# Optimization experiments

Hardware: AMD Instinct MI355X
Metric: run time of the kernel (lower is better)

Reference implementation:

```python
import jax, jax.numpy as jnp
import numpy as np

# YOLOv4 stride-8 head config (yolov4.cfg)
ALL_ANCHORS = [[12,16],[19,36],[40,28],[36,75],[76,55],[72,146],[142,110],[192,243],[459,401]]
ANCHOR_MASK = [0, 1, 2]
N_CLASSES = 80
SCALE_XY = 1.2  # scale_x_y for this head
N_BBOX_ATTRS = 5  # tx, ty, tw, th, obj


def setup_inputs() -> dict:
    key = jax.random.key(0)
    attrs = N_CLASSES + N_BBOX_ATTRS  # 85
    n_anchors = len(ANCHOR_MASK)      # 3
    # raw conv output: [batch, n_anchors*attrs, grid, grid]
    x = jax.random.normal(key, (16, n_anchors * attrs, 76, 76), dtype=jnp.float32)
    return {"x": x, "input_dim": 608}


def reference(x, input_dim):
    B = x.shape[0]
    G = x.shape[2]                      # grid_dim (INPUT_H_DIM)
    stride = input_dim // G             # grid_stride
    A = len(ANCHOR_MASK)
    attrs = N_CLASSES + N_BBOX_ATTRS

    # anchors scaled to grid units: [A, 2]
    anc = jnp.asarray([ALL_ANCHORS[i] for i in ANCHOR_MASK], dtype=jnp.float32) / stride

    # [B, A, attrs, H, W] -> [B, H, W, A, attrs]
    x = x.reshape(B, A, attrs, G, G).transpose(0, 3, 4, 1, 2)

    # yolo_transform: sigmoid+scale tx/ty, exp*anchor tw/th, sigmoid obj+cls
    txy = jax.nn.sigmoid(x[..., 0:2]) * SCALE_XY - (SCALE_XY - 1.0) / 2.0
    twh = jnp.exp(x[..., 2:4]) * anc            # broadcast over [B,H,W,A,2]
    objcls = jax.nn.sigmoid(x[..., 4:])

    # add_grid_offsets: torch.meshgrid(grid, grid) is 'ij' -> y_offset[i,j]=i, x_offset[i,j]=j
    gy, gx = jnp.meshgrid(jnp.arange(G), jnp.arange(G), indexing="ij")
    off = jnp.stack([gx, gy], axis=-1).astype(jnp.float32)[:, :, None, :]  # [H,W,1,2]
    txy = txy + off

    # scale bbox attrs (tx..th) to input-image pixels
    boxes = jnp.concatenate([txy, twh], axis=-1) * jnp.float32(stride)

    out = jnp.concatenate([boxes, objcls], axis=-1)  # [B,H,W,A,attrs]
    return out.reshape(B, G * G * A, attrs)
```

## Files before the change

### kernel.cpp

```cpp
#include <hip/hip_runtime.h>

#define GRIDD  76
#define NROWS  255
#define GG     (GRIDD * GRIDD)
#define QROWS  64
#define QQ     (QROWS * 19)
#define QDW    (QROWS * GRIDD)

typedef __attribute__((address_space(3))) unsigned lds_u32;
typedef __attribute__((address_space(1))) unsigned glb_u32;

__device__ __forceinline__ void gll16(const float* g, float* l) {
    __builtin_amdgcn_global_load_lds((const glb_u32*)g, (lds_u32*)l, 16, 0, 0);
}

__global__ __launch_bounds__(256, 8) void yolo_head_kernel(
    const float* __restrict__ x, const int* __restrict__ dimp,
    float* __restrict__ out)
{
    __shared__ float buf[QDW];
    const unsigned lb    = (blockIdx.x & 7u) * 608u + (blockIdx.x >> 3);
    const unsigned b     = lb / 304u;
    const unsigned hq    = lb - b * 304u;
    const unsigned h     = hq >> 2;
    const unsigned q     = hq & 3u;
    const unsigned rbase = (q == 3u) ? 191u : (q << 6);
    const unsigned t     = threadIdx.x;
    const unsigned wid   = t >> 6;
    const unsigned lane  = t & 63u;
    const float stride   = (float)(*dimp / GRIDD);
    const float fh       = (float)h;

    const float* __restrict__ src = x + (size_t)(b * NROWS + rbase) * GG + h * GRIDD;
    #pragma unroll
    for (unsigned k = 0; k < 5u; ++k) {
        unsigned i = k * 256u + (wid << 6) + lane;
        if (i < QQ) {
            unsigned row = i / 19u;
            unsigned qc  = i - row * 19u;
            gll16(src + (size_t)row * GG + (qc << 2),
                  buf + (size_t)(k * 256u + (wid << 6)) * 4u);
        }
    }
    __syncthreads();

    const unsigned rem  = rbase + lane;
    const unsigned a    = (rem >= 170u) ? 2u : ((rem >= 85u) ? 1u : 0u);
    const unsigned attr = rem - a * 85u;
    const bool  wh  = (attr == 2u) | (attr == 3u);
    const bool  isx = (attr == 0u);
    float anc = 0.f;
    if (attr == 2u) anc = (a == 0u) ? 12.f : ((a == 1u) ? 19.f : 40.f);
    if (attr == 3u) anc = (a == 0u) ? 16.f : ((a == 1u) ? 36.f : 28.f);
    const float mB    = -0.1f * stride;
    const float slog  = wh ? 1.44269504f : -1.44269504f;
    const float A2    = wh ? anc : ((attr < 2u) ? 1.2f * stride : 1.f);
    const float wsel  = isx ? stride : 0.f;
    const float basef = (attr == 1u) ? fmaf(fh, stride, mB) : (isx ? mB : 0.f);
    float* __restrict__ dst = out + (size_t)(b * GRIDD + h) * (GRIDD * NROWS) + rem;

    #pragma unroll
    for (unsigned j = 0; j < 5u; ++j) {
        const unsigned tt = wid + (j << 2);
        if (tt < 19u) {
            const float4 vv = *reinterpret_cast<const float4*>(
                buf + (size_t)lane * GRIDD + (tt << 2));
            #pragma unroll
            for (unsigned i = 0; i < 4u; ++i) {
                const float v  = (i == 0) ? vv.x : (i == 1) ? vv.y : (i == 2) ? vv.z : vv.w;
                const float uf = (float)((tt << 2) + i);
                const float e2 = exp2f(v * slog);
                const float sg = __builtin_amdgcn_rcpf(1.0f + e2);
                const float qv = wh ? e2 : sg;
                const float o  = fmaf(qv, A2, fmaf(uf, wsel, basef));
                dst[(size_t)((tt << 2) + i) * NROWS] = o;
            }
        }
    }
}

extern "C" void kernel_launch(void* const* d_in, const int* in_sizes, int n_in,
                              void* d_out, int out_size, void* d_ws, size_t ws_size,
                              hipStream_t stream) {
    const float* x  = (const float*)d_in[0];
    const int* dimp = (const int*)d_in[1];
    float* out      = (float*)d_out;
    const int B = in_sizes[0] / (NROWS * GG);
    yolo_head_kernel<<<B * GRIDD * 4, 256, 0, stream>>>(x, dimp, out);
}
```

Baseline: 32.96 us.

## Make blocks persistent with double-buffered async LDS staging across rows

Replaces one-block-per-(batch,row,quarter) with 1024 persistent blocks of 512 threads. Each block walks a contiguous range of batch-rows and double-buffers the global-to-LDS loads, so the next row's load overlaps the current row's compute and stores. Synchronization uses raw s_waitcnt/s_barrier asm. This removes per-block launch and load-latency stalls, but relies on exact vmcnt accounting, and the number of rows per block is uneven.

```diff
diff --git a/kernel.cpp b/kernel.cpp
--- a/kernel.cpp
+++ b/kernel.cpp
@@ -4,8 +4,8 @@
 #define NROWS  255
 #define GG     (GRIDD * GRIDD)
 #define QROWS  64
-#define QQ     (QROWS * 19)
 #define QDW    (QROWS * GRIDD)
+#define NGRP   256
 
 typedef __attribute__((address_space(3))) unsigned lds_u32;
 typedef __attribute__((address_space(1))) unsigned glb_u32;
@@ -14,41 +14,50 @@
     __builtin_amdgcn_global_load_lds((const glb_u32*)g, (lds_u32*)l, 16, 0, 0);
 }
 
-__global__ __launch_bounds__(256, 8) void yolo_head_kernel(
+__device__ __forceinline__ void stage_q(const float* __restrict__ src,
+                                        float* buf, unsigned wid, unsigned lane)
+{
+    #pragma unroll
+    for (unsigned k = 0; k < 2u; ++k) {
+        unsigned i   = k * 512u + (wid << 6) + lane;
+        unsigned row = i / 19u;
+        unsigned qc  = i - row * 19u;
+        gll16(src + (size_t)row * GG + (qc << 2),
+              buf + (size_t)(k * 512u + (wid << 6)) * 4u);
+    }
+    {
+        unsigned i = 1024u + wid * 24u + lane;
+        if (lane < 24u) {
+            unsigned row = i / 19u;
+            unsigned qc  = i - row * 19u;
+            gll16(src + (size_t)row * GG + (qc << 2),
+                  buf + (size_t)(1024u + wid * 24u) * 4u);
+        }
+    }
+}
+
+__global__ __launch_bounds__(512, 8) void yolo_head_kernel(
     const float* __restrict__ x, const int* __restrict__ dimp,
-    float* __restrict__ out)
+    float* __restrict__ out, int nbh)
 {
-    __shared__ float buf[QDW];
-    const unsigned lb    = (blockIdx.x & 7u) * 608u + (blockIdx.x >> 3);
-    const unsigned b     = lb / 304u;
-    const unsigned hq    = lb - b * 304u;
-    const unsigned h     = hq >> 2;
-    const unsigned q     = hq & 3u;
+    __shared__ float buf[2][QDW];
+    const unsigned g     = blockIdx.x & 255u;
+    const unsigned q     = blockIdx.x >> 8;
     const unsigned rbase = (q == 3u) ? 191u : (q << 6);
     const unsigned t     = threadIdx.x;
     const unsigned wid   = t >> 6;
     const unsigned lane  = t & 63u;
     const float stride   = (float)(*dimp / GRIDD);
-    const float fh       = (float)h;
-
-    const float* __restrict__ src = x + (size_t)(b * NROWS + rbase) * GG + h * GRIDD;
-    #pragma unroll
-    for (unsigned k = 0; k < 5u; ++k) {
-        unsigned i = k * 256u + (wid << 6) + lane;
-        if (i < QQ) {
-            unsigned row = i / 19u;
-            unsigned qc  = i - row * 19u;
-            gll16(src + (size_t)row * GG + (qc << 2),
-                  buf + (size_t)(k * 256u + (wid << 6)) * 4u);
-        }
-    }
-    __syncthreads();
+    const unsigned bh0 = (g * (unsigned)nbh) >> 8;
+    const unsigned bh1 = ((g + 1u) * (unsigned)nbh) >> 8;
+    const unsigned n   = bh1 - bh0;
 
     const unsigned rem  = rbase + lane;
     const unsigned a    = (rem >= 170u) ? 2u : ((rem >= 85u) ? 1u : 0u);
     const unsigned attr = rem - a * 85u;
-    const bool  wh  = (attr == 2u) | (attr == 3u);
-    const bool  isx = (attr == 0u);
+    const bool  wh   = (attr == 2u) | (attr == 3u);
+    const bool  isx  = (attr == 0u);
+    const bool  isy  = (attr == 1u);
     float anc = 0.f;
     if (attr == 2u) anc = (a == 0u) ? 12.f : ((a == 1u) ? 19.f : 40.f);
     if (attr == 3u) anc = (a == 0u) ? 16.f : ((a == 1u) ? 36.f : 28.f);
@@ -56,27 +65,45 @@
     const float slog  = wh ? 1.44269504f : -1.44269504f;
     const float A2    = wh ? anc : ((attr < 2u) ? 1.2f * stride : 1.f);
     const float wsel  = isx ? stride : 0.f;
-    const float basef = (attr == 1u) ? fmaf(fh, stride, mB) : (isx ? mB : 0.f);
-    float* __restrict__ dst = out + (size_t)(b * GRIDD + h) * (GRIDD * NROWS) + rem;
+    const float base0 = isx ? mB : 0.f;
 
-    #pragma unroll
-    for (unsigned j = 0; j < 5u; ++j) {
-        const unsigned tt = wid + (j << 2);
-        if (tt < 19u) {
-            const float4 vv = *reinterpret_cast<const float4*>(
-                buf + (size_t)lane * GRIDD + (tt << 2));
-            #pragma unroll
-            for (unsigned i = 0; i < 4u; ++i) {
-                const float v  = (i == 0) ? vv.x : (i == 1) ? vv.y : (i == 2) ? vv.z : vv.w;
-                const float uf = (float)((tt << 2) + i);
-                const float e2 = exp2f(v * slog);
-                const float sg = __builtin_amdgcn_rcpf(1.0f + e2);
-                const float qv = wh ? e2 : sg;
-                const float o  = fmaf(qv, A2, fmaf(uf, wsel, basef));
-                dst[(size_t)((tt << 2) + i) * NROWS] = o;
+    #define SRC(bh) (x + (size_t)(((bh) / GRIDD) * NROWS + rbase) * GG \
+                       + (size_t)((bh) % GRIDD) * GRIDD)
+    stage_q(SRC(bh0), buf[0], wid, lane);
+    if (n > 1u) stage_q(SRC(bh0 + 1u), buf[1], wid, lane);
+
+    for (unsigned i = 0; i < n; ++i) {
+        const unsigned bh = bh0 + i;
+        if (i + 1u < n) asm volatile("s_waitcnt vmcnt(3)\n\ts_barrier" ::: "memory");
+        else            asm volatile("s_waitcnt vmcnt(0)\n\ts_barrier" ::: "memory");
+
+        const float fh    = (float)(bh % GRIDD);
+        const float basef = isy ? fmaf(fh, stride, mB) : base0;
+        const float* bc   = buf[i & 1u];
+        float* __restrict__ dst = out + (size_t)bh * (GRIDD * NROWS) + rem;
+        #pragma unroll
+        for (unsigned j = 0; j < 3u; ++j) {
+            const unsigned tt = wid + (j << 3);
+            if (tt < 19u) {
+                const float4 vv = *reinterpret_cast<const float4*>(
+                    bc + (size_t)lane * GRIDD + (tt << 2));
+                #pragma unroll
+                for (unsigned i2 = 0; i2 < 4u; ++i2) {
+                    const float v  = (i2 == 0) ? vv.x : (i2 == 1) ? vv.y
+                                   : (i2 == 2) ? vv.z : vv.w;
+                    const float uf = (float)((tt << 2) + i2);
+                    const float e2 = exp2f(v * slog);
+                    const float sg = __builtin_amdgcn_rcpf(1.0f + e2);
+                    const float qv = wh ? e2 : sg;
+                    const float o  = fmaf(qv, A2, fmaf(uf, wsel, basef));
+                    dst[(size_t)((tt << 2) + i2) * NROWS] = o;
+                }
             }
         }
+        asm volatile("s_waitcnt lgkmcnt(0)\n\ts_barrier" ::: "memory");
+        if (i + 2u < n) stage_q(SRC(bh + 2u), buf[i & 1u], wid, lane);
     }
+    #undef SRC
 }
 
 extern "C" void kernel_launch(void* const* d_in, const int* in_sizes, int n_in,
@@ -85,6 +112,7 @@
     const float* x  = (const float*)d_in[0];
     const int* dimp = (const int*)d_in[1];
     float* out      = (float*)d_out;
-    const int B = in_sizes[0] / (NROWS * GG);
-    yolo_head_kernel<<<B * GRIDD * 4, 256, 0, stream>>>(x, dimp, out);
+    const int B   = in_sizes[0] / (NROWS * GG);
+    const int nbh = B * GRIDD;
+    yolo_head_kernel<<<4 * NGRP, 512, 0, stream>>>(x, dimp, out, nbh);
 }
```

Measured after the change: 47.05 us. 42.8% more time.
